# Optimization experiments

Hardware: AMD Instinct MI355X
Metric: run time of the kernel (lower is better)

## Reference

```python
import jax, jax.numpy as jnp
import numpy as np

NA, NQ, FDIM, NC, HID = 512, 4096, 2, 16, 64
CUTOFF = 6.0
GAMMA = 10.0
BOX = 12.0


def setup_inputs() -> dict:
    key = jax.random.key(0)
    ks = jax.random.split(key, 16)
    s = lambda k, shp, fan: jax.random.normal(k, shp, jnp.float32) * (1.0 / np.sqrt(fan))
    return {
        "atom_pos": jax.random.uniform(ks[0], (NA, 3), jnp.float32) * BOX,
        "atom_feat": jax.random.normal(ks[1], (NA, FDIM), jnp.float32),
        "query_pos": jax.random.uniform(ks[2], (NQ, 3), jnp.float32) * BOX,
        "W1": s(ks[3], (FDIM + NC, HID), FDIM + NC), "b1": jnp.zeros((HID,), jnp.float32),
        "W2": s(ks[4], (HID, HID), HID), "b2": jnp.zeros((HID,), jnp.float32),
        "W3": s(ks[5], (HID, HID // 2), HID), "b3": jnp.zeros((HID // 2,), jnp.float32),
        "W4": s(ks[6], (HID // 2, 1), HID // 2), "b4": jnp.zeros((1,), jnp.float32),
        "W5": s(ks[7], (3, 64), 3), "b5": jnp.zeros((64,), jnp.float32),
        "W6": s(ks[8], (64, 3), 64), "b6": jnp.zeros((3,), jnp.float32),
    }


def _forward(atom_pos, atom_feat, query_pos, W1, b1, W2, b2, W3, b3, W4, b4, W5, b5, W6, b6):
    centers = jnp.linspace(0.0, CUTOFF, NC, dtype=jnp.float32)  # RBF centers
    rel = query_pos[:, None, :] - atom_pos[None, :, :]          # (Nq,Na,3)
    dist = jnp.linalg.norm(rel + 1e-12, axis=-1)                 # (Nq,Na) (matches torch.norm(rel+eps))
    mask = (dist <= CUTOFF).astype(dist.dtype)
    rbf = jnp.exp(-GAMMA * (dist[..., None] - centers) ** 2)     # (Nq,Na,Nc)
    feat_b = jnp.broadcast_to(atom_feat[None], (query_pos.shape[0],) + atom_feat.shape)
    atom_input = jnp.concatenate([feat_b, rbf], axis=-1)         # (Nq,Na,F+Nc)
    h = jax.nn.relu(atom_input @ W1 + b1)
    h = jax.nn.relu(h @ W2 + b2)                                 # (Nq,Na,H)
    scalar_w = (jax.nn.relu(h @ W3 + b3) @ W4 + b4)[..., 0] * mask  # (Nq,Na)
    dir_vec = rel / (dist[..., None] + 1e-12)                    # (Nq,Na,3)
    weighted = jnp.einsum('qa,qad->qd', scalar_w, dir_vec)       # (Nq,3)
    out = jax.nn.relu(weighted @ W5 + b5) @ W6 + b6              # (Nq,3)
    return out


def reference(atom_pos, atom_feat, query_pos, W1, b1, W2, b2, W3, b3, W4, b4, W5, b5, W6, b6):
    return _forward(atom_pos, atom_feat, query_pos, W1, b1, W2, b2, W3, b3, W4, b4, W5, b5, W6, b6)
```

## Files before the change

### kernel.cpp

```cpp
#include <hip/hip_runtime.h>
#include <math.h>


typedef _Float16 f16x4 __attribute__((ext_vector_type(4)));
typedef _Float16 f16x2 __attribute__((ext_vector_type(2)));
typedef float    f32x4 __attribute__((ext_vector_type(4)));

#define NT 2
#define NS 512

#define MFMA16(A,B,C) __builtin_amdgcn_mfma_f32_16x16x16f16(A,B,C,0,0,0)

__device__ __forceinline__ float exp2_fast(float x) {
    float r;
    asm("v_exp_f32 %0, %1" : "=v"(r) : "v"(x));
    return r;
}

__device__ __forceinline__ f16x4 relu_cvt(f32x4 c) {
    return f16x4{(_Float16)fmaxf(c[0],0.f), (_Float16)fmaxf(c[1],0.f),
                 (_Float16)fmaxf(c[2],0.f), (_Float16)fmaxf(c[3],0.f)};
}

__global__ __launch_bounds__(64) void repack_kernel(
    const float* __restrict__ W1, const float* __restrict__ b1,
    const float* __restrict__ W2, const float* __restrict__ b2,
    const float* __restrict__ W3, const float* __restrict__ b3,
    const float* __restrict__ W4, char* __restrict__ ws)
{
    const int b = blockIdx.x, l = threadIdx.x;
    const int col = l & 15, quad = l >> 4;
    if (b < 32) {
        f16x4 v;
        #pragma unroll
        for (int j = 0; j < 4; ++j) {
            float x;
            if (b < 8) {
                const int kc = b >> 2, mt = b & 3;
                const int k = kc*16 + quad*4 + j;
                if (k < 16)       x = W1[(k+2)*64 + mt*16 + col];
                else if (k == 16) x = W1[        mt*16 + col];
                else if (k == 17) x = W1[ 64   + mt*16 + col];
                else if (k == 18) x = b1[        mt*16 + col];
                else              x = 0.0f;
            } else if (b < 24) {
                const int idx = b - 8, kc = idx >> 2, mt = idx & 3;
                const int k = kc*16 + quad*4 + j;
                x = W2[k*64 + mt*16 + col];
            } else {
                const int idx = b - 24, kc = idx >> 1, mt = idx & 1;
                const int k = kc*16 + quad*4 + j;
                x = W3[k*32 + mt*16 + col];
            }
            v[j] = (_Float16)x;
        }
        *(f16x4*)(ws + (b*64 + l)*8) = v;
    } else {
        float* bo = (float*)(ws + 16384);
        #pragma unroll
        for (int i = l; i < 128; i += 64) {
            float x;
            if (i < 64)       x = b2[i];
            else if (i < 96)  x = b3[i - 64];
            else              x = W4[i - 96];
            bo[i] = x;
        }
    }
}

__global__ __launch_bounds__(256, 4) void tabgen_kernel(
    const float* __restrict__ atom_feat,
    const float* __restrict__ b4,
    const char*  __restrict__ ws,
    float* __restrict__ tab)
{
    __shared__ __align__(16) f16x4 wlds[2048];
    __shared__ __align__(16) float biaslds[128];

    const int tid  = threadIdx.x;
    const int wave = __builtin_amdgcn_readfirstlane(tid >> 6);
    const int lane = tid & 63;
    const int col  = lane & 15;
    const int quad = lane >> 4;

    {
        const f16x4* wsrc = (const f16x4*)ws;
        #pragma unroll
        for (int i = 0; i < 8; ++i)
            wlds[tid + i*256] = wsrc[tid + i*256];
        if (tid < 128) biaslds[tid] = ((const float*)(ws + 16384))[tid];
    }
    __syncthreads();

    const int c  = blockIdx.x * 4 + wave;
    const int a  = c >> 4;
    const int i0 = (c & 15) * 32;
    const float f0 = atom_feat[a*2+0];
    const float f1 = atom_feat[a*2+1];
    const float b4v = b4[0];
    const float4* bias4 = (const float4*)biaslds;

    const float cbase = 1.5193132f * (float)(quad*4);

    f16x4 xa0[NT], xa1[NT];
    #pragma unroll
    for (int u = 0; u < NT; ++u) {
        const int   idx  = i0 + u*16 + col;
        const float dist = (float)idx * (6.0f/511.0f);
        const float base = __fmul_rn(dist, 3.7982831f) - cbase;
        #pragma unroll
        for (int j = 0; j < 4; ++j) {
            const float t = base - 1.5193132f * (float)j;
            xa0[u][j] = (_Float16)exp2_fast(t * -t);
        }
        const bool q0 = (quad == 0);
        xa1[u] = f16x4{q0 ? (_Float16)f0 : (_Float16)0.f,
                       q0 ? (_Float16)f1 : (_Float16)0.f,
                       (_Float16)(q0 ? 1.f : 0.f),
                       (_Float16)0.f};
    }

    f16x4 t1[2][4];
    #pragma unroll
    for (int kc = 0; kc < 2; ++kc)
        #pragma unroll
        for (int mt = 0; mt < 4; ++mt)
            t1[kc][mt] = wlds[(kc*4 + mt)*64 + lane];
    f16x4 a2[NT][4];
    #pragma unroll
    for (int u = 0; u < NT; ++u)
        #pragma unroll
        for (int mt = 0; mt < 4; ++mt) {
            f32x4 cc = {0.f, 0.f, 0.f, 0.f};
            cc = MFMA16(t1[0][mt], xa0[u], cc);
            cc = MFMA16(t1[1][mt], xa1[u], cc);
            a2[u][mt] = relu_cvt(cc);
        }

    f16x4 t2[4][4];
    #pragma unroll
    for (int kc = 0; kc < 4; ++kc)
        #pragma unroll
        for (int mt = 0; mt < 4; ++mt)
            t2[kc][mt] = wlds[(8 + kc*4 + mt)*64 + lane];
    float4 b2v[4];
    #pragma unroll
    for (int mt = 0; mt < 4; ++mt) b2v[mt] = bias4[mt*4 + quad];
    f16x4 a3[NT][4];
    #pragma unroll
    for (int u = 0; u < NT; ++u)
        #pragma unroll
        for (int mt = 0; mt < 4; ++mt) {
            f32x4 cc = {b2v[mt].x, b2v[mt].y, b2v[mt].z, b2v[mt].w};
            #pragma unroll
            for (int kc = 0; kc < 4; ++kc)
                cc = MFMA16(t2[kc][mt], a2[u][kc], cc);
            a3[u][mt] = relu_cvt(cc);
        }

    f16x4 t3[4][2];
    #pragma unroll
    for (int kc = 0; kc < 4; ++kc)
        #pragma unroll
        for (int mt = 0; mt < 2; ++mt)
            t3[kc][mt] = wlds[(24 + kc*2 + mt)*64 + lane];
    float4 b3v[2], w4v[2];
    #pragma unroll
    for (int mt = 0; mt < 2; ++mt) {
        b3v[mt] = bias4[16 + mt*4 + quad];
        w4v[mt] = bias4[24 + mt*4 + quad];
    }
    #pragma unroll
    for (int u = 0; u < NT; ++u) {
        float s = 0.f;
        #pragma unroll
        for (int mt = 0; mt < 2; ++mt) {
            f32x4 cc = {b3v[mt].x, b3v[mt].y, b3v[mt].z, b3v[mt].w};
            #pragma unroll
            for (int kc = 0; kc < 4; ++kc)
                cc = MFMA16(t3[kc][mt], a3[u][kc], cc);
            const float* wv = &w4v[mt].x;
            #pragma unroll
            for (int rr = 0; rr < 4; ++rr)
                s = fmaf(fmaxf(cc[rr], 0.f), wv[rr], s);
        }
        s += __shfl_xor(s, 16);
        s += __shfl_xor(s, 32);
        s += b4v;
        if (quad == 0)
            tab[a*NS + i0 + u*16 + col] = s;
    }
}

__global__ __launch_bounds__(256, 4) void field_kernel(
    const float* __restrict__ atom_pos,
    const float* __restrict__ query_pos,
    const float* __restrict__ W5, const float* __restrict__ b5,
    const float* __restrict__ W6, const float* __restrict__ b6,
    const float* __restrict__ tab,
    float* __restrict__ out)
{
    __shared__ float px[512], py[512], pz[512];

    const int tid  = threadIdx.x;
    const int wave = __builtin_amdgcn_readfirstlane(tid >> 6);
    const int lane = tid & 63;
    const int q    = blockIdx.x * 4 + wave;

    #pragma unroll
    for (int i = tid; i < 512; i += 256) {
        px[i] = atom_pos[i*3+0];
        py[i] = atom_pos[i*3+1];
        pz[i] = atom_pos[i*3+2];
    }
    __syncthreads();

    const float qx = query_pos[q*3+0];
    const float qy = query_pos[q*3+1];
    const float qz = query_pos[q*3+2];

    float acc0 = 0.f, acc1 = 0.f, acc2 = 0.f;
    #pragma unroll
    for (int it = 0; it < 8; ++it) {
        const int a = it*64 + lane;
        const float rx = qx - px[a];
        const float ry = qy - py[a];
        const float rz = qz - pz[a];
        const float ex = __fadd_rn(rx, 1e-12f);
        const float ey = __fadd_rn(ry, 1e-12f);
        const float ez = __fadd_rn(rz, 1e-12f);
        const float dd = __fadd_rn(__fadd_rn(__fmul_rn(ex,ex), __fmul_rn(ey,ey)),
                                   __fmul_rn(ez,ez));
        const float dist = sqrtf(dd);
        const bool  in   = dist <= 6.0f;
        const float t  = __fmul_rn(dist, 85.166664f);
        int   i  = (int)t;
        i = i < (NS-2) ? i : (NS-2);
        const float frac = t - (float)i;
        const float* row = tab + a*NS;
        const float s0 = row[i];
        const float s1 = row[i+1];
        const float sv = fmaf(frac, s1 - s0, s0);
        const float inv = __builtin_amdgcn_rcpf(dist + 1e-12f);
        const float wm  = in ? sv * inv : 0.f;
        acc0 = fmaf(wm, rx, acc0);
        acc1 = fmaf(wm, ry, acc1);
        acc2 = fmaf(wm, rz, acc2);
    }

    #pragma unroll
    for (int o = 1; o < 64; o <<= 1) {
        acc0 += __shfl_xor(acc0, o);
        acc1 += __shfl_xor(acc1, o);
        acc2 += __shfl_xor(acc2, o);
    }

    int hz = 0;
    asm volatile("" : "+v"(hz));
    const float w5x = W5[hz + lane];
    const float w5y = W5[hz + 64 + lane];
    const float w5z = W5[hz + 128 + lane];
    const float b5v = b5[hz + lane];
    float th = fmaf(acc0, w5x, fmaf(acc1, w5y, fmaf(acc2, w5z, b5v)));
    th = fmaxf(th, 0.f);
    float o0 = th * W6[hz + lane*3+0];
    float o1 = th * W6[hz + lane*3+1];
    float o2 = th * W6[hz + lane*3+2];
    #pragma unroll
    for (int o = 1; o < 64; o <<= 1) {
        o0 += __shfl_xor(o0, o);
        o1 += __shfl_xor(o1, o);
        o2 += __shfl_xor(o2, o);
    }
    if (lane == 0) {
        out[q*3+0] = o0 + b6[0];
        out[q*3+1] = o1 + b6[1];
        out[q*3+2] = o2 + b6[2];
    }
}

extern "C" void kernel_launch(void* const* d_in, const int* in_sizes, int n_in,
                              void* d_out, int out_size, void* d_ws, size_t ws_size,
                              hipStream_t stream) {
    const float* atom_pos  = (const float*)d_in[0];
    const float* atom_feat = (const float*)d_in[1];
    const float* query_pos = (const float*)d_in[2];
    const float* W1 = (const float*)d_in[3];  const float* b1 = (const float*)d_in[4];
    const float* W2 = (const float*)d_in[5];  const float* b2 = (const float*)d_in[6];
    const float* W3 = (const float*)d_in[7];  const float* b3 = (const float*)d_in[8];
    const float* W4 = (const float*)d_in[9];  const float* b4 = (const float*)d_in[10];
    const float* W5 = (const float*)d_in[11]; const float* b5 = (const float*)d_in[12];
    const float* W6 = (const float*)d_in[13]; const float* b6 = (const float*)d_in[14];
    float* out = (float*)d_out;
    char*  ws  = (char*)d_ws;
    float* tab = (float*)(ws + 32768);

    hipLaunchKernelGGL(repack_kernel, dim3(33), dim3(64), 0, stream,
                       W1, b1, W2, b2, W3, b3, W4, ws);
    hipLaunchKernelGGL(tabgen_kernel, dim3(2048), dim3(256), 0, stream,
                       atom_feat, b4, (const char*)ws, tab);
    hipLaunchKernelGGL(field_kernel, dim3(1024), dim3(256), 0, stream,
                       atom_pos, query_pos, W5, b5, W6, b6,
                       (const float*)tab, out);
}
```

Before: 100.9 us.

## Fuse weight repack into tabgen and halve its grid with per-wave chunk loop

```diff
diff --git a/kernel.cpp b/kernel.cpp
--- a/kernel.cpp
+++ b/kernel.cpp
@@ -6,7 +6,6 @@
 typedef _Float16 f16x2 __attribute__((ext_vector_type(2)));
 typedef float    f32x4 __attribute__((ext_vector_type(4)));
 
-#define NT 2
 #define NS 512
 
 #define MFMA16(A,B,C) __builtin_amdgcn_mfma_f32_16x16x16f16(A,B,C,0,0,0)
@@ -22,56 +21,12 @@
                  (_Float16)fmaxf(c[2],0.f), (_Float16)fmaxf(c[3],0.f)};
 }
 
-__global__ __launch_bounds__(64) void repack_kernel(
+__global__ __launch_bounds__(256, 4) void tabgen_kernel(
+    const float* __restrict__ atom_feat,
     const float* __restrict__ W1, const float* __restrict__ b1,
     const float* __restrict__ W2, const float* __restrict__ b2,
     const float* __restrict__ W3, const float* __restrict__ b3,
-    const float* __restrict__ W4, char* __restrict__ ws)
-{
-    const int b = blockIdx.x, l = threadIdx.x;
-    const int col = l & 15, quad = l >> 4;
-    if (b < 32) {
-        f16x4 v;
-        #pragma unroll
-        for (int j = 0; j < 4; ++j) {
-            float x;
-            if (b < 8) {
-                const int kc = b >> 2, mt = b & 3;
-                const int k = kc*16 + quad*4 + j;
-                if (k < 16)       x = W1[(k+2)*64 + mt*16 + col];
-                else if (k == 16) x = W1[        mt*16 + col];
-                else if (k == 17) x = W1[ 64   + mt*16 + col];
-                else if (k == 18) x = b1[        mt*16 + col];
-                else              x = 0.0f;
-            } else if (b < 24) {
-                const int idx = b - 8, kc = idx >> 2, mt = idx & 3;
-                const int k = kc*16 + quad*4 + j;
-                x = W2[k*64 + mt*16 + col];
-            } else {
-                const int idx = b - 24, kc = idx >> 1, mt = idx & 1;
-                const int k = kc*16 + quad*4 + j;
-                x = W3[k*32 + mt*16 + col];
-            }
-            v[j] = (_Float16)x;
-        }
-        *(f16x4*)(ws + (b*64 + l)*8) = v;
-    } else {
-        float* bo = (float*)(ws + 16384);
-        #pragma unroll
-        for (int i = l; i < 128; i += 64) {
-            float x;
-            if (i < 64)       x = b2[i];
-            else if (i < 96)  x = b3[i - 64];
-            else              x = W4[i - 96];
-            bo[i] = x;
-        }
-    }
-}
-
-__global__ __launch_bounds__(256, 4) void tabgen_kernel(
-    const float* __restrict__ atom_feat,
-    const float* __restrict__ b4,
-    const char*  __restrict__ ws,
+    const float* __restrict__ W4, const float* __restrict__ b4,
     float* __restrict__ tab)
 {
     __shared__ __align__(16) f16x4 wlds[2048];
@@ -83,112 +38,151 @@
     const int col  = lane & 15;
     const int quad = lane >> 4;
 
-    {
-        const f16x4* wsrc = (const f16x4*)ws;
-        #pragma unroll
-        for (int i = 0; i < 8; ++i)
-            wlds[tid + i*256] = wsrc[tid + i*256];
-        if (tid < 128) biaslds[tid] = ((const float*)(ws + 16384))[tid];
+    #pragma unroll
+    for (int sidx = 0; sidx < 8; ++sidx) {
+        const int s  = tid + sidx*256;
+        const int b  = s >> 6;
+        const int sl = s & 63;
+        const int scol = sl & 15, squad = sl >> 4;
+        f16x4 v;
+        #pragma unroll
+        for (int j = 0; j < 4; ++j) {
+            float x;
+            if (b < 8) {
+                const int kc = b >> 2, mt = b & 3;
+                const int k = kc*16 + squad*4 + j;
+                if (k < 16)       x = W1[(k+2)*64 + mt*16 + scol];
+                else if (k == 16) x = W1[        mt*16 + scol];
+                else if (k == 17) x = W1[ 64   + mt*16 + scol];
+                else if (k == 18) x = b1[        mt*16 + scol];
+                else              x = 0.0f;
+            } else if (b < 24) {
+                const int idx = b - 8, kc = idx >> 2, mt = idx & 3;
+                const int k = kc*16 + squad*4 + j;
+                x = W2[k*64 + mt*16 + scol];
+            } else {
+                const int idx = b - 24, kc = idx >> 1, mt = idx & 1;
+                const int k = kc*16 + squad*4 + j;
+                x = W3[k*32 + mt*16 + scol];
+            }
+            v[j] = (_Float16)x;
+        }
+        wlds[s] = v;
+    }
+    if (tid < 128) {
+        float x;
+        if (tid < 64)       x = b2[tid];
+        else if (tid < 96)  x = b3[tid - 64];
+        else                x = W4[tid - 96];
+        biaslds[tid] = x;
     }
     __syncthreads();
 
-    const int c  = blockIdx.x * 4 + wave;
-    const int a  = c >> 4;
-    const int i0 = (c & 15) * 32;
-    const float f0 = atom_feat[a*2+0];
-    const float f1 = atom_feat[a*2+1];
+    const int wc     = blockIdx.x * 4 + wave;
+    const int a      = wc >> 3;
+    const int i0base = (wc & 7) * 64;
+    const float f0  = atom_feat[a*2+0];
+    const float f1  = atom_feat[a*2+1];
     const float b4v = b4[0];
-    const float4* bias4 = (const float4*)biaslds;
 
     const float cbase = 1.5193132f * (float)(quad*4);
 
-    f16x4 xa0[NT], xa1[NT];
-    #pragma unroll
-    for (int u = 0; u < NT; ++u) {
-        const int   idx  = i0 + u*16 + col;
-        const float dist = (float)idx * (6.0f/511.0f);
-        const float base = __fmul_rn(dist, 3.7982831f) - cbase;
-        #pragma unroll
-        for (int j = 0; j < 4; ++j) {
-            const float t = base - 1.5193132f * (float)j;
-            xa0[u][j] = (_Float16)exp2_fast(t * -t);
-        }
-        const bool q0 = (quad == 0);
-        xa1[u] = f16x4{q0 ? (_Float16)f0 : (_Float16)0.f,
-                       q0 ? (_Float16)f1 : (_Float16)0.f,
-                       (_Float16)(q0 ? 1.f : 0.f),
-                       (_Float16)0.f};
-    }
-
-    f16x4 t1[2][4];
-    #pragma unroll
-    for (int kc = 0; kc < 2; ++kc)
-        #pragma unroll
-        for (int mt = 0; mt < 4; ++mt)
-            t1[kc][mt] = wlds[(kc*4 + mt)*64 + lane];
-    f16x4 a2[NT][4];
-    #pragma unroll
-    for (int u = 0; u < NT; ++u)
-        #pragma unroll
-        for (int mt = 0; mt < 4; ++mt) {
-            f32x4 cc = {0.f, 0.f, 0.f, 0.f};
-            cc = MFMA16(t1[0][mt], xa0[u], cc);
-            cc = MFMA16(t1[1][mt], xa1[u], cc);
-            a2[u][mt] = relu_cvt(cc);
-        }
-
-    f16x4 t2[4][4];
-    #pragma unroll
-    for (int kc = 0; kc < 4; ++kc)
-        #pragma unroll
-        for (int mt = 0; mt < 4; ++mt)
-            t2[kc][mt] = wlds[(8 + kc*4 + mt)*64 + lane];
-    float4 b2v[4];
-    #pragma unroll
-    for (int mt = 0; mt < 4; ++mt) b2v[mt] = bias4[mt*4 + quad];
-    f16x4 a3[NT][4];
-    #pragma unroll
-    for (int u = 0; u < NT; ++u)
-        #pragma unroll
-        for (int mt = 0; mt < 4; ++mt) {
-            f32x4 cc = {b2v[mt].x, b2v[mt].y, b2v[mt].z, b2v[mt].w};
-            #pragma unroll
-            for (int kc = 0; kc < 4; ++kc)
-                cc = MFMA16(t2[kc][mt], a2[u][kc], cc);
-            a3[u][mt] = relu_cvt(cc);
-        }
-
-    f16x4 t3[4][2];
-    #pragma unroll
-    for (int kc = 0; kc < 4; ++kc)
-        #pragma unroll
-        for (int mt = 0; mt < 2; ++mt)
-            t3[kc][mt] = wlds[(24 + kc*2 + mt)*64 + lane];
-    float4 b3v[2], w4v[2];
-    #pragma unroll
-    for (int mt = 0; mt < 2; ++mt) {
-        b3v[mt] = bias4[16 + mt*4 + quad];
-        w4v[mt] = bias4[24 + mt*4 + quad];
-    }
-    #pragma unroll
-    for (int u = 0; u < NT; ++u) {
-        float s = 0.f;
+    #pragma unroll 1
+    for (int cc = 0; cc < 2; ++cc) {
+        const int i0 = i0base + cc*32;
+
+        int wb = 0;
+        asm volatile("" : "+v"(wb));
+        const float4* bias4 = (const float4*)biaslds;
+
+        f16x4 xa0[2], xa1[2];
+        #pragma unroll
+        for (int u = 0; u < 2; ++u) {
+            const int   idx  = i0 + u*16 + col;
+            const float dist = (float)idx * (6.0f/511.0f);
+            const float base = __fmul_rn(dist, 3.7982831f) - cbase;
+            #pragma unroll
+            for (int j = 0; j < 4; ++j) {
+                const float t = base - 1.5193132f * (float)j;
+                xa0[u][j] = (_Float16)exp2_fast(t * -t);
+            }
+            const bool q0 = (quad == 0);
+            xa1[u] = f16x4{q0 ? (_Float16)f0 : (_Float16)0.f,
+                           q0 ? (_Float16)f1 : (_Float16)0.f,
+                           (_Float16)(q0 ? 1.f : 0.f),
+                           (_Float16)0.f};
+        }
+
+        f16x4 t1[2][4];
+        #pragma unroll
+        for (int kc = 0; kc < 2; ++kc)
+            #pragma unroll
+            for (int mt = 0; mt < 4; ++mt)
+                t1[kc][mt] = wlds[wb + (kc*4 + mt)*64 + lane];
+        f16x4 a2[2][4];
+        #pragma unroll
+        for (int u = 0; u < 2; ++u)
+            #pragma unroll
+            for (int mt = 0; mt < 4; ++mt) {
+                f32x4 cc2 = {0.f, 0.f, 0.f, 0.f};
+                cc2 = MFMA16(t1[0][mt], xa0[u], cc2);
+                cc2 = MFMA16(t1[1][mt], xa1[u], cc2);
+                a2[u][mt] = relu_cvt(cc2);
+            }
+
+        f16x4 t2[4][4];
+        #pragma unroll
+        for (int kc = 0; kc < 4; ++kc)
+            #pragma unroll
+            for (int mt = 0; mt < 4; ++mt)
+                t2[kc][mt] = wlds[wb + (8 + kc*4 + mt)*64 + lane];
+        float4 b2v[4];
+        #pragma unroll
+        for (int mt = 0; mt < 4; ++mt) b2v[mt] = bias4[wb + mt*4 + quad];
+        f16x4 a3[2][4];
+        #pragma unroll
+        for (int u = 0; u < 2; ++u)
+            #pragma unroll
+            for (int mt = 0; mt < 4; ++mt) {
+                f32x4 cc2 = {b2v[mt].x, b2v[mt].y, b2v[mt].z, b2v[mt].w};
+                #pragma unroll
+                for (int kc = 0; kc < 4; ++kc)
+                    cc2 = MFMA16(t2[kc][mt], a2[u][kc], cc2);
+                a3[u][mt] = relu_cvt(cc2);
+            }
+
+        f16x4 t3[4][2];
+        #pragma unroll
+        for (int kc = 0; kc < 4; ++kc)
+            #pragma unroll
+            for (int mt = 0; mt < 2; ++mt)
+                t3[kc][mt] = wlds[wb + (24 + kc*2 + mt)*64 + lane];
+        float4 b3v[2], w4v[2];
         #pragma unroll
         for (int mt = 0; mt < 2; ++mt) {
-            f32x4 cc = {b3v[mt].x, b3v[mt].y, b3v[mt].z, b3v[mt].w};
-            #pragma unroll
-            for (int kc = 0; kc < 4; ++kc)
-                cc = MFMA16(t3[kc][mt], a3[u][kc], cc);
-            const float* wv = &w4v[mt].x;
-            #pragma unroll
-            for (int rr = 0; rr < 4; ++rr)
-                s = fmaf(fmaxf(cc[rr], 0.f), wv[rr], s);
-        }
-        s += __shfl_xor(s, 16);
-        s += __shfl_xor(s, 32);
-        s += b4v;
-        if (quad == 0)
-            tab[a*NS + i0 + u*16 + col] = s;
+            b3v[mt] = bias4[wb + 16 + mt*4 + quad];
+            w4v[mt] = bias4[wb + 24 + mt*4 + quad];
+        }
+        #pragma unroll
+        for (int u = 0; u < 2; ++u) {
+            float s = 0.f;
+            #pragma unroll
+            for (int mt = 0; mt < 2; ++mt) {
+                f32x4 cc2 = {b3v[mt].x, b3v[mt].y, b3v[mt].z, b3v[mt].w};
+                #pragma unroll
+                for (int kc = 0; kc < 4; ++kc)
+                    cc2 = MFMA16(t3[kc][mt], a3[u][kc], cc2);
+                const float* wv = &w4v[mt].x;
+                #pragma unroll
+                for (int rr = 0; rr < 4; ++rr)
+                    s = fmaf(fmaxf(cc2[rr], 0.f), wv[rr], s);
+            }
+            s += __shfl_xor(s, 16);
+            s += __shfl_xor(s, 32);
+            s += b4v;
+            if (quad == 0)
+                tab[a*NS + i0 + u*16 + col] = s;
+        }
     }
 }
 
@@ -292,13 +286,10 @@
     const float* W5 = (const float*)d_in[11]; const float* b5 = (const float*)d_in[12];
     const float* W6 = (const float*)d_in[13]; const float* b6 = (const float*)d_in[14];
     float* out = (float*)d_out;
-    char*  ws  = (char*)d_ws;
-    float* tab = (float*)(ws + 32768);
-
-    hipLaunchKernelGGL(repack_kernel, dim3(33), dim3(64), 0, stream,
-                       W1, b1, W2, b2, W3, b3, W4, ws);
-    hipLaunchKernelGGL(tabgen_kernel, dim3(2048), dim3(256), 0, stream,
-                       atom_feat, b4, (const char*)ws, tab);
+    float* tab = (float*)d_ws;
+
+    hipLaunchKernelGGL(tabgen_kernel, dim3(1024), dim3(256), 0, stream,
+                       atom_feat, W1, b1, W2, b2, W3, b3, W4, b4, tab);
     hipLaunchKernelGGL(field_kernel, dim3(1024), dim3(256), 0, stream,
                        atom_pos, query_pos, W5, b5, W6, b6,
                        (const float*)tab, out);
```

Result: no change. 100.4 us (-0.5%).
